# Optimization experiments

Measured on AMD Instinct MI355X. Metric: run time of the kernel, lower is better.

The kernel has to match this reference:

```python
import jax, jax.numpy as jnp
import numpy as np

NUM_BINS = 1000
VALUE_MAX = 10.0
SMOOTH = 5
EPS = 1e-08


def _smooth(x):
    # x: (B, L, T) -> moving average over bins dim, kernel=SMOOTH, stride=1
    if SMOOTH <= 1:
        return x
    c = jnp.cumsum(x, axis=1)
    c = jnp.concatenate([jnp.zeros_like(c[:, :1]), c], axis=1)  # (B, L+1, T)
    return (c[:, SMOOTH:] - c[:, :-SMOOTH]) / SMOOTH  # (B, L-SMOOTH+1, T)


def _digitize(v, edges):
    # torch.bucketize(values, edges[1:-1]) with right=False == searchsorted side='left'
    v = jnp.clip(v, 0.0, VALUE_MAX - EPS)
    return jnp.searchsorted(edges[1:-1], v, side='left')


def setup_inputs() -> dict:
    key = jax.random.key(0)
    k1, k2 = jax.random.split(key)
    y_pred = jax.random.normal(k1, (8, 8192, 32), dtype=jnp.float32)
    y_true = jax.random.normal(k2, (8, 8192, 32), dtype=jnp.float32)
    return {"y_pred": y_pred, "y_true": y_true}


def reference(y_pred, y_true):
    edges = jnp.linspace(0.0, VALUE_MAX, NUM_BINS + 1)
    ps = _smooth(y_pred.astype(jnp.float32))
    ts = _smooth(y_true.astype(jnp.float32))
    B, L, T = ps.shape
    pf = ps.reshape(-1, T)  # (N, T), N = B*L
    tf = ts.reshape(-1, T)
    valid = jnp.isfinite(pf) & jnp.isfinite(tf)
    pf = jnp.where(valid, pf, 0.0)
    tf = jnp.where(valid, tf, 0.0)
    pb = _digitize(pf, edges)  # (N, T) int bin ids in [0, NUM_BINS)
    tb = _digitize(tf, edges)
    w = valid.astype(jnp.int32)  # invalid samples contribute 0 counts
    tr = jnp.broadcast_to(jnp.arange(T)[None, :], pb.shape)  # track id per sample
    pred_hist = jnp.zeros((T, NUM_BINS), jnp.int32).at[tr, pb].add(w)
    target_hist = jnp.zeros((T, NUM_BINS), jnp.int32).at[tr, tb].add(w)
    joint_hist = jnp.zeros((T, NUM_BINS, NUM_BINS), jnp.int32).at[tr, pb, tb].add(w)
    return pred_hist, target_hist, joint_hist
```

## Files before the change

kernel.cpp:

```cpp
#include <hip/hip_runtime.h>

typedef unsigned int uint_t;

#define LL 8192
#define TT 32
#define NGPB 2047
#define NGROUPS (8 * NGPB)
#define NSAMP 65504
#define KSTRIDE 65536
#define NBINS 1000
#define K1_BLOCKS 512
#define OV_CAP 8
#define HSTRIDE 260
#define NHIST 128
#define NZERO 1920
#define REGION_A 5952000
#define REGION_TOT 7475712
#define WS_CNT_OFF 0
#define WS_REC_OFF 512
#define WS_KEYS_INT_OFF 16384
#define WS_NEEDED ((size_t)(WS_KEYS_INT_OFF + (size_t)TT * KSTRIDE) * 4)

__device__ __forceinline__ int bin_of(float v) {
    v = fminf(fmaxf(v, 0.0f), 10.0f);
    int b = (int)ceilf(v * 100.0f) - 1;
    b = b < 0 ? 0 : b;
    return b > (NBINS - 1) ? (NBINS - 1) : b;
}

__global__ __launch_bounds__(512) void k1_bin(
    const float* __restrict__ yp, const float* __restrict__ yt,
    int* __restrict__ out, int* __restrict__ ws)
{
    __shared__ int s_ovc;
    const int tid = threadIdx.x;
    const int bid = blockIdx.x;
    if (tid == 0) s_ovc = 0;

    if (tid < 125) out[bid * 125 + tid] = 0;
    __syncthreads();

    uint_t* __restrict__ keys = (uint_t*)(ws + WS_KEYS_INT_OFF);
    const int trk   = tid & 31;
    const int slotg = tid >> 5;

    #pragma unroll
    for (int pass = 0; pass < 2; ++pass) {
        const int g = bid * 32 + pass * 16 + slotg;
        if (g >= NGROUPS) continue;
        const int b = g / NGPB;
        const int j = g - b * NGPB;
        const size_t base = ((size_t)b * LL + 4 * (size_t)j) * TT + trk;
        float xp[8], xt[8];
        #pragma unroll
        for (int k = 0; k < 8; ++k) {
            xp[k] = yp[base + (size_t)k * TT];
            xt[k] = yt[base + (size_t)k * TT];
        }
        uint_t kk[4];
        #pragma unroll
        for (int r = 0; r < 4; ++r) {
            const float ps = (xp[r]+xp[r+1]+xp[r+2]+xp[r+3]+xp[r+4]) * 0.2f;
            const float ts = (xt[r]+xt[r+1]+xt[r+2]+xt[r+3]+xt[r+4]) * 0.2f;
            uint_t key = 0xFFFFFFFFu;
            if (isfinite(ps) && isfinite(ts)) {
                const int pb = bin_of(ps);
                const int tb = bin_of(ts);
                key = ((uint_t)pb << 10) | (uint_t)tb;
                if (pb >= 256 || tb >= 256) {
                    const int idx = atomicAdd(&s_ovc, 1);
                    if (idx < OV_CAP)
                        ws[WS_REC_OFF + bid * OV_CAP + idx] = (trk << 20) | (pb << 10) | tb;
                }
            }
            kk[r] = key;
        }
        *(uint4*)&keys[(size_t)trk * KSTRIDE + (size_t)g * 4] =
            make_uint4(kk[0], kk[1], kk[2], kk[3]);
    }

    __syncthreads();
    if (tid == 0) ws[WS_CNT_OFF + bid] = min(s_ovc, OV_CAP);
}

__global__ __launch_bounds__(512) void k2_main(
    const int* __restrict__ ws, int* __restrict__ out)
{
    extern __shared__ int hist[];
    const int tid = threadIdx.x;
    const int bid = blockIdx.x;

    int* __restrict__ pred_g  = out;
    int* __restrict__ targ_g  = out + TT * NBINS;
    int* __restrict__ joint_g = out + 2 * TT * NBINS;

    if (bid < NHIST) {
        const int t  = bid & 31;
        const int q  = bid >> 5;
        const int r0 = q * 64;
        int* __restrict__ joint_t = joint_g + (size_t)t * NBINS * NBINS;
        const uint_t* __restrict__ kt =
            (const uint_t*)(ws + WS_KEYS_INT_OFF) + (size_t)t * KSTRIDE;

        for (int i = tid; i < 64 * HSTRIDE; i += 512) hist[i] = 0;
        __syncthreads();

        int c00 = 0;
        #pragma unroll 4
        for (int p = 0; p < 32; ++p) {
            const int i4 = tid + p * 512;
            if (i4 < NGROUPS) {
                const uint4 w = *(const uint4*)&kt[i4 * 4];
                const uint_t ks[4] = {w.x, w.y, w.z, w.w};
                #pragma unroll
                for (int h = 0; h < 4; ++h) {
                    const uint_t key = ks[h];
                    const uint_t tb  = key & 1023u;
                    const uint_t rr  = (key >> 10) - (uint_t)r0;
                    if (rr < 64u && tb < 256u) {
                        if (key == 0u) c00++;
                        else atomicAdd(&hist[rr * HSTRIDE + tb], 1);
                    }
                }
            }
        }
        if (c00) atomicAdd(&hist[0], c00);
        __syncthreads();

        for (int i = tid; i < 64 * 64; i += 512) {
            const int r  = i >> 6;
            const int c4 = i & 63;
            *(int4*)&joint_t[(size_t)(r0 + r) * NBINS + c4 * 4] =
                *(const int4*)&hist[r * HSTRIDE + c4 * 4];
        }
        {
            const int r = tid >> 3, s = tid & 7;
            int sum = 0;
            #pragma unroll
            for (int k = 0; k < 32; ++k)
                sum += hist[r * HSTRIDE + s * 32 + ((k + tid) & 31)];
            sum += __shfl_xor(sum, 1);
            sum += __shfl_xor(sum, 2);
            sum += __shfl_xor(sum, 4);
            if (s == 0) pred_g[t * NBINS + r0 + r] = sum;
        }
        {
            const int c = tid >> 1, u = tid & 1;
            int sum = 0;
            #pragma unroll
            for (int r = 0; r < 32; ++r)
                sum += hist[(u * 32 + r) * HSTRIDE + c];
            sum += __shfl_xor(sum, 1);
            if (u == 0 && sum) atomicAdd(&targ_g[t * NBINS + c], sum);
        }
    } else {
        int4* __restrict__ j4 = (int4*)joint_g;
        const int start = (bid - NHIST) * 512 + tid;
        for (int v = start; v < REGION_TOT; v += NZERO * 512) {
            int4* dst;
            if (v < REGION_A) {
                const int trk2 = v / 186000;
                const int rem  = v - trk2 * 186000;
                dst = j4 + (size_t)trk2 * 250000 + 64000 + rem;
            } else {
                const int w2   = v - REGION_A;
                const int trk2 = w2 / 47616;
                const int rem  = w2 - trk2 * 47616;
                const int r    = rem / 186;
                const int c4   = rem - r * 186;
                dst = j4 + (size_t)trk2 * 250000 + r * 250 + 64 + c4;
            }
            *dst = make_int4(0, 0, 0, 0);
        }
    }
}

__global__ __launch_bounds__(256) void k3_patch(
    const int* __restrict__ ws, int* __restrict__ out)
{
    int* __restrict__ pred_g  = out;
    int* __restrict__ targ_g  = out + TT * NBINS;
    int* __restrict__ joint_g = out + 2 * TT * NBINS;
    for (int b = threadIdx.x; b < K1_BLOCKS; b += 256) {
        const int cnt = ws[WS_CNT_OFF + b];
        for (int k = 0; k < cnt; ++k) {
            const int rec = ws[WS_REC_OFF + b * OV_CAP + k];
            const int trk = rec >> 20;
            const int pb  = (rec >> 10) & 1023;
            const int tb  = rec & 1023;
            atomicAdd(&joint_g[(size_t)trk * NBINS * NBINS + pb * NBINS + tb], 1);
            atomicAdd(&pred_g[trk * NBINS + pb], 1);
            atomicAdd(&targ_g[trk * NBINS + tb], 1);
        }
    }
}

__global__ __launch_bounds__(256) void fb_zero(int4* __restrict__ p, int n4) {
    const int i = blockIdx.x * 256 + threadIdx.x;
    if (i < n4) p[i] = make_int4(0, 0, 0, 0);
}

__global__ __launch_bounds__(512) void fb_hist(
    const float* __restrict__ yp, const float* __restrict__ yt,
    int* __restrict__ out)
{
    __shared__ int s_h[16 * 1009];
    const int tid = threadIdx.x;
    const int trk = tid & 15;
    const int slot = tid >> 4;
    const int t = blockIdx.y * 16 + trk;

    for (int i = tid; i < 16 * 1009; i += 512) s_h[i] = 0;
    __syncthreads();
    int* __restrict__ reg = &s_h[trk * 1009];
    int* __restrict__ pred_g  = out;
    int* __restrict__ targ_g  = out + TT * NBINS;
    int* __restrict__ joint_g = out + 2 * TT * NBINS;
    int* __restrict__ joint_t = joint_g + (size_t)t * NBINS * NBINS;
    int c00 = 0, cp0 = 0, ct0 = 0;
    const int g0 = blockIdx.x * 128;
    #pragma unroll
    for (int pass = 0; pass < 4; ++pass) {
        const int g = g0 + pass * 32 + slot;
        if (g < NGROUPS) {
            const int b = g / NGPB;
            const int j = g - b * NGPB;
            const size_t base = ((size_t)b * LL + 4 * (size_t)j) * TT + t;
            float xp[8], xt[8];
            #pragma unroll
            for (int k = 0; k < 8; ++k) {
                xp[k] = yp[base + (size_t)k * TT];
                xt[k] = yt[base + (size_t)k * TT];
            }
            #pragma unroll
            for (int r = 0; r < 4; ++r) {
                const float ps = (xp[r]+xp[r+1]+xp[r+2]+xp[r+3]+xp[r+4]) * 0.2f;
                const float ts = (xt[r]+xt[r+1]+xt[r+2]+xt[r+3]+xt[r+4]) * 0.2f;
                if (!(isfinite(ps) && isfinite(ts))) continue;
                const int pb = bin_of(ps);
                const int tb = bin_of(ts);
                if (pb == 0) cp0++;
                else if (pb < 136) atomicAdd(&reg[736 + pb], 1);
                else atomicAdd(&pred_g[t * NBINS + pb], 1);
                if (tb == 0) ct0++;
                else if (tb < 136) atomicAdd(&reg[872 + tb], 1);
                else atomicAdd(&targ_g[t * NBINS + tb], 1);
                if (pb == 0 && tb == 0) c00++;
                else if (pb < 16 && tb < 16) atomicAdd(&reg[pb * 16 + tb], 1);
                else if (pb == 0 && tb < 256) atomicAdd(&reg[256 + tb - 16], 1);
                else if (tb == 0 && pb < 256) atomicAdd(&reg[496 + pb - 16], 1);
                else atomicAdd(&joint_t[pb * NBINS + tb], 1);
            }
        }
    }
    if (c00) atomicAdd(&reg[0],   c00);
    if (cp0) atomicAdd(&reg[736], cp0);
    if (ct0) atomicAdd(&reg[872], ct0);
    __syncthreads();
    const int h0 = blockIdx.y * 16;
    for (int i = tid; i < 16 * 1008; i += 512) {
        const int tr = i / 1008;
        const int sl = i - tr * 1008;
        const int c  = s_h[tr * 1009 + sl];
        if (c == 0) continue;
        const int tg = h0 + tr;
        if (sl < 256) atomicAdd(&joint_g[(size_t)tg * NBINS * NBINS + (sl >> 4) * NBINS + (sl & 15)], c);
        else if (sl < 496) atomicAdd(&joint_g[(size_t)tg * NBINS * NBINS + (sl - 240)], c);
        else if (sl < 736) atomicAdd(&joint_g[(size_t)tg * NBINS * NBINS + (size_t)(sl - 480) * NBINS], c);
        else if (sl < 872) atomicAdd(&pred_g[tg * NBINS + (sl - 736)], c);
        else atomicAdd(&targ_g[tg * NBINS + (sl - 872)], c);
    }
}

extern "C" void kernel_launch(void* const* d_in, const int* in_sizes, int n_in,
                              void* d_out, int out_size, void* d_ws, size_t ws_size,
                              hipStream_t stream) {
    const float* yp = (const float*)d_in[0];
    const float* yt = (const float*)d_in[1];
    int* out = (int*)d_out;

    if (ws_size >= WS_NEEDED) {
        int* ws = (int*)d_ws;
        k1_bin<<<K1_BLOCKS, 512, 0, stream>>>(yp, yt, out, ws);
        k2_main<<<NHIST + NZERO, 512, 64 * HSTRIDE * sizeof(int), stream>>>(ws, out);
        k3_patch<<<1, 256, 0, stream>>>(ws, out);
    } else {
        const int n4 = out_size / 4;
        fb_zero<<<(n4 + 255) / 256, 256, 0, stream>>>((int4*)out, n4);
        dim3 grid((NGROUPS + 127) / 128, 2);
        fb_hist<<<grid, 512, 0, stream>>>(yp, yt, out);
    }
}
```

Before: 40.31 us.

## Merge patch kernel into k2 via last-block atomic counter and split zeroing

Removes the separate single-block overflow-patch kernel: each k2 block increments a done counter after a threadfence, and the last block to finish applies the overflow records. Zeroing of the joint histogram is split so that k1 clears the first part of the region after binning and k2 clears the rest with far fewer blocks (512 in total instead of 2048). This saves one kernel launch and tail, and moves some store traffic into k1. In exchange, k1 does more work and the last-block pattern serialises the patch step at the end of k2.

```diff
diff --git a/kernel.cpp b/kernel.cpp
--- a/kernel.cpp
+++ b/kernel.cpp
@@ -6,18 +6,20 @@
 #define TT 32
 #define NGPB 2047
 #define NGROUPS (8 * NGPB)
-#define NSAMP 65504
 #define KSTRIDE 65536
 #define NBINS 1000
 #define K1_BLOCKS 512
 #define OV_CAP 8
 #define HSTRIDE 260
 #define NHIST 128
-#define NZERO 1920
+#define K2_BLOCKS 512
+#define NZERO (K2_BLOCKS - NHIST)
 #define REGION_A 5952000
 #define REGION_TOT 7475712
+#define ZA 3600000
 #define WS_CNT_OFF 0
 #define WS_REC_OFF 512
+#define WS_DONE_OFF 8192
 #define WS_KEYS_INT_OFF 16384
 #define WS_NEEDED ((size_t)(WS_KEYS_INT_OFF + (size_t)TT * KSTRIDE) * 4)
 
@@ -26,6 +28,21 @@
     int b = (int)ceilf(v * 100.0f) - 1;
     b = b < 0 ? 0 : b;
     return b > (NBINS - 1) ? (NBINS - 1) : b;
+}
+
+__device__ __forceinline__ int4* zaddr(int4* __restrict__ j4, int v) {
+    if (v < REGION_A) {
+        const int trk = v / 186000;
+        const int rem = v - trk * 186000;
+        return j4 + (size_t)trk * 250000 + 64000 + rem;
+    } else {
+        const int w   = v - REGION_A;
+        const int trk = w / 47616;
+        const int rem = w - trk * 47616;
+        const int r   = rem / 186;
+        const int c4  = rem - r * 186;
+        return j4 + (size_t)trk * 250000 + r * 250 + 64 + c4;
+    }
 }
 
 __global__ __launch_bounds__(512) void k1_bin(
@@ -35,8 +52,10 @@
     __shared__ int s_ovc;
     const int tid = threadIdx.x;
     const int bid = blockIdx.x;
-    if (tid == 0) s_ovc = 0;
-
+    if (tid == 0) {
+        s_ovc = 0;
+        if (bid == 0) ws[WS_DONE_OFF] = 0;
+    }
     if (tid < 125) out[bid * 125 + tid] = 0;
     __syncthreads();
 
@@ -81,12 +100,17 @@
 
     __syncthreads();
     if (tid == 0) ws[WS_CNT_OFF + bid] = min(s_ovc, OV_CAP);
+
+    int4* __restrict__ j4 = (int4*)(out + 2 * TT * NBINS);
+    for (int v = bid * 512 + tid; v < ZA; v += K1_BLOCKS * 512)
+        *zaddr(j4, v) = make_int4(0, 0, 0, 0);
 }
 
 __global__ __launch_bounds__(512) void k2_main(
-    const int* __restrict__ ws, int* __restrict__ out)
+    int* __restrict__ ws, int* __restrict__ out)
 {
     extern __shared__ int hist[];
+    __shared__ int s_old;
     const int tid = threadIdx.x;
     const int bid = blockIdx.x;
 
@@ -155,36 +179,20 @@
         }
     } else {
         int4* __restrict__ j4 = (int4*)joint_g;
-        const int start = (bid - NHIST) * 512 + tid;
-        for (int v = start; v < REGION_TOT; v += NZERO * 512) {
-            int4* dst;
-            if (v < REGION_A) {
-                const int trk2 = v / 186000;
-                const int rem  = v - trk2 * 186000;
-                dst = j4 + (size_t)trk2 * 250000 + 64000 + rem;
-            } else {
-                const int w2   = v - REGION_A;
-                const int trk2 = w2 / 47616;
-                const int rem  = w2 - trk2 * 47616;
-                const int r    = rem / 186;
-                const int c4   = rem - r * 186;
-                dst = j4 + (size_t)trk2 * 250000 + r * 250 + 64 + c4;
-            }
-            *dst = make_int4(0, 0, 0, 0);
-        }
-    }
-}
-
-__global__ __launch_bounds__(256) void k3_patch(
-    const int* __restrict__ ws, int* __restrict__ out)
-{
-    int* __restrict__ pred_g  = out;
-    int* __restrict__ targ_g  = out + TT * NBINS;
-    int* __restrict__ joint_g = out + 2 * TT * NBINS;
-    for (int b = threadIdx.x; b < K1_BLOCKS; b += 256) {
-        const int cnt = ws[WS_CNT_OFF + b];
+        for (int v = ZA + (bid - NHIST) * 512 + tid; v < REGION_TOT; v += NZERO * 512)
+            *zaddr(j4, v) = make_int4(0, 0, 0, 0);
+    }
+
+    __syncthreads();
+    if (tid == 0) {
+        __threadfence();
+        s_old = atomicAdd(&ws[WS_DONE_OFF], 1);
+    }
+    __syncthreads();
+    if (s_old == K2_BLOCKS - 1) {
+        const int cnt = ws[WS_CNT_OFF + tid];
         for (int k = 0; k < cnt; ++k) {
-            const int rec = ws[WS_REC_OFF + b * OV_CAP + k];
+            const int rec = ws[WS_REC_OFF + tid * OV_CAP + k];
             const int trk = rec >> 20;
             const int pb  = (rec >> 10) & 1023;
             const int tb  = rec & 1023;
@@ -282,8 +290,7 @@
     if (ws_size >= WS_NEEDED) {
         int* ws = (int*)d_ws;
         k1_bin<<<K1_BLOCKS, 512, 0, stream>>>(yp, yt, out, ws);
-        k2_main<<<NHIST + NZERO, 512, 64 * HSTRIDE * sizeof(int), stream>>>(ws, out);
-        k3_patch<<<1, 256, 0, stream>>>(ws, out);
+        k2_main<<<K2_BLOCKS, 512, 64 * HSTRIDE * sizeof(int), stream>>>(ws, out);
     } else {
         const int n4 = out_size / 4;
         fb_zero<<<(n4 + 255) / 256, 256, 0, stream>>>((int4*)out, n4);
```

Measured after the change: 56.32 us. 1.4x slower.

## Pack joint histogram as 16-bit pairs, two blocks per track, fewer zero blocks

Applied to the files above, without the earlier changes.

Each histogram block now covers all 256 pred rows for one 128-column half of the track's dense corner, with two 16-bit counters packed per LDS word so the 256x128 tile fits in shared memory. This halves the histogram blocks from 128 to 64, so each track's key stream is scanned twice instead of four times. The zero-fill grid shrinks from 1920 to 448 blocks and the address math moves into a helper. Pred sums now go through atomics and target sums through plain stores; the packed 16-bit counters would overflow if any single bin exceeded 65535 counts.

```diff
diff --git a/kernel.cpp b/kernel.cpp
--- a/kernel.cpp
+++ b/kernel.cpp
@@ -5,15 +5,15 @@
 #define LL 8192
 #define TT 32
 #define NGPB 2047
-#define NGROUPS (8 * NGPB)
-#define NSAMP 65504
+#define NGROUPS 16376
 #define KSTRIDE 65536
 #define NBINS 1000
 #define K1_BLOCKS 512
 #define OV_CAP 8
-#define HSTRIDE 260
-#define NHIST 128
-#define NZERO 1920
+#define SQW 65
+#define NHIST 64
+#define K2_BLOCKS 512
+#define NZB (K2_BLOCKS - NHIST)
 #define REGION_A 5952000
 #define REGION_TOT 7475712
 #define WS_CNT_OFF 0
@@ -28,6 +28,21 @@
     return b > (NBINS - 1) ? (NBINS - 1) : b;
 }
 
+__device__ __forceinline__ int4* zaddr(int4* __restrict__ j4, int v) {
+    if (v < REGION_A) {
+        const int trk = v / 186000;
+        const int rem = v - trk * 186000;
+        return j4 + (size_t)trk * 250000 + 64000 + rem;
+    } else {
+        const int w   = v - REGION_A;
+        const int trk = w / 47616;
+        const int rem = w - trk * 47616;
+        const int r   = rem / 186;
+        const int c4  = rem - r * 186;
+        return j4 + (size_t)trk * 250000 + r * 250 + 64 + c4;
+    }
+}
+
 __global__ __launch_bounds__(512) void k1_bin(
     const float* __restrict__ yp, const float* __restrict__ yt,
     int* __restrict__ out, int* __restrict__ ws)
@@ -36,7 +51,6 @@
     const int tid = threadIdx.x;
     const int bid = blockIdx.x;
     if (tid == 0) s_ovc = 0;
-
     if (tid < 125) out[bid * 125 + tid] = 0;
     __syncthreads();
 
@@ -86,7 +100,7 @@
 __global__ __launch_bounds__(512) void k2_main(
     const int* __restrict__ ws, int* __restrict__ out)
 {
-    extern __shared__ int hist[];
+    extern __shared__ uint_t lds[];
     const int tid = threadIdx.x;
     const int bid = blockIdx.x;
 
@@ -95,14 +109,13 @@
     int* __restrict__ joint_g = out + 2 * TT * NBINS;
 
     if (bid < NHIST) {
-        const int t  = bid & 31;
-        const int q  = bid >> 5;
-        const int r0 = q * 64;
+        const int t    = bid & 31;
+        const int half = bid >> 5;
         int* __restrict__ joint_t = joint_g + (size_t)t * NBINS * NBINS;
         const uint_t* __restrict__ kt =
             (const uint_t*)(ws + WS_KEYS_INT_OFF) + (size_t)t * KSTRIDE;
 
-        for (int i = tid; i < 64 * HSTRIDE; i += 512) hist[i] = 0;
+        for (int i = tid; i < 256 * SQW; i += 512) lds[i] = 0;
         __syncthreads();
 
         int c00 = 0;
@@ -115,63 +128,52 @@
                 #pragma unroll
                 for (int h = 0; h < 4; ++h) {
                     const uint_t key = ks[h];
-                    const uint_t tb  = key & 1023u;
-                    const uint_t rr  = (key >> 10) - (uint_t)r0;
-                    if (rr < 64u && tb < 256u) {
-                        if (key == 0u) c00++;
-                        else atomicAdd(&hist[rr * HSTRIDE + tb], 1);
-                    }
+                    if ((key & 0x000C0300u) != 0u) continue;
+                    const uint_t tb = key & 1023u;
+                    if ((int)(tb >> 7) != half) continue;
+                    if (key == 0u) { c00++; continue; }
+                    const uint_t pb = key >> 10;
+                    atomicAdd(&lds[pb * SQW + ((tb & 127u) >> 1)],
+                              1u << ((tb & 1u) << 4));
                 }
             }
         }
-        if (c00) atomicAdd(&hist[0], c00);
+        if (c00) atomicAdd(&lds[0], (uint_t)c00);
         __syncthreads();
 
-        for (int i = tid; i < 64 * 64; i += 512) {
-            const int r  = i >> 6;
-            const int c4 = i & 63;
-            *(int4*)&joint_t[(size_t)(r0 + r) * NBINS + c4 * 4] =
-                *(const int4*)&hist[r * HSTRIDE + c4 * 4];
-        }
-        {
-            const int r = tid >> 3, s = tid & 7;
+        for (int i = tid; i < 256 * 32; i += 512) {
+            const int r  = i >> 5;
+            const int c4 = i & 31;
+            const uint_t w0 = lds[r * SQW + c4 * 2];
+            const uint_t w1 = lds[r * SQW + c4 * 2 + 1];
+            *(int4*)&joint_t[(size_t)r * NBINS + half * 128 + c4 * 4] =
+                make_int4(w0 & 0xFFFFu, w0 >> 16, w1 & 0xFFFFu, w1 >> 16);
+        }
+
+        if (tid < 256) {
             int sum = 0;
-            #pragma unroll
-            for (int k = 0; k < 32; ++k)
-                sum += hist[r * HSTRIDE + s * 32 + ((k + tid) & 31)];
+            #pragma unroll 8
+            for (int w = 0; w < 64; ++w) {
+                const uint_t x = lds[tid * SQW + w];
+                sum += (int)(x & 0xFFFFu) + (int)(x >> 16);
+            }
+            if (sum) atomicAdd(&pred_g[t * NBINS + tid], sum);
+        } else {
+            const int c = (tid - 256) >> 1;
+            const int u = tid & 1;
+            int sum = 0;
+            #pragma unroll 8
+            for (int k = 0; k < 128; ++k) {
+                const int r = u * 128 + k;
+                sum += (int)((lds[r * SQW + (c >> 1)] >> ((c & 1) << 4)) & 0xFFFFu);
+            }
             sum += __shfl_xor(sum, 1);
-            sum += __shfl_xor(sum, 2);
-            sum += __shfl_xor(sum, 4);
-            if (s == 0) pred_g[t * NBINS + r0 + r] = sum;
-        }
-        {
-            const int c = tid >> 1, u = tid & 1;
-            int sum = 0;
-            #pragma unroll
-            for (int r = 0; r < 32; ++r)
-                sum += hist[(u * 32 + r) * HSTRIDE + c];
-            sum += __shfl_xor(sum, 1);
-            if (u == 0 && sum) atomicAdd(&targ_g[t * NBINS + c], sum);
+            if (u == 0) targ_g[t * NBINS + half * 128 + c] = sum;
         }
     } else {
         int4* __restrict__ j4 = (int4*)joint_g;
-        const int start = (bid - NHIST) * 512 + tid;
-        for (int v = start; v < REGION_TOT; v += NZERO * 512) {
-            int4* dst;
-            if (v < REGION_A) {
-                const int trk2 = v / 186000;
-                const int rem  = v - trk2 * 186000;
-                dst = j4 + (size_t)trk2 * 250000 + 64000 + rem;
-            } else {
-                const int w2   = v - REGION_A;
-                const int trk2 = w2 / 47616;
-                const int rem  = w2 - trk2 * 47616;
-                const int r    = rem / 186;
-                const int c4   = rem - r * 186;
-                dst = j4 + (size_t)trk2 * 250000 + r * 250 + 64 + c4;
-            }
-            *dst = make_int4(0, 0, 0, 0);
-        }
+        for (int v = (bid - NHIST) * 512 + tid; v < REGION_TOT; v += NZB * 512)
+            *zaddr(j4, v) = make_int4(0, 0, 0, 0);
     }
 }
 
@@ -282,7 +284,7 @@
     if (ws_size >= WS_NEEDED) {
         int* ws = (int*)d_ws;
         k1_bin<<<K1_BLOCKS, 512, 0, stream>>>(yp, yt, out, ws);
-        k2_main<<<NHIST + NZERO, 512, 64 * HSTRIDE * sizeof(int), stream>>>(ws, out);
+        k2_main<<<K2_BLOCKS, 512, 256 * SQW * sizeof(uint_t), stream>>>(ws, out);
         k3_patch<<<1, 256, 0, stream>>>(ws, out);
     } else {
         const int n4 = out_size / 4;
```

New measurement: 50.12 us. +24.4%, slower.
